# Kernel tuning notes

Hardware: AMD Instinct MI355X
Metric: run time of the kernel (lower is better)

The kernel has to match this reference:

```python
import jax, jax.numpy as jnp
import numpy as np

# Math note: torch does fold(unfold(low_fea,k,pad) * repeat_c(unfold(kernel,1))).
# Because the unfolded low_fea entry at patch (i,j), offset (a,b) is low_fea[c, i-pad+a, j-pad+b],
# fold's overlap-add collapses to: out[n,c,y,x] = low_fea[n,c,y,x] * S[n,y,x], where
#   S[n,y,x] = sum_{a,b in [0,k)} kernel[n, a*k+b, y+pad-a, x+pad-b]  (zero outside bounds).
# We compute S with a zero-padded shifted sum (k*k small static loop) instead of
# materializing the k2*c*h*w unfolded tensor.


def setup_inputs() -> dict:
    key = jax.random.key(0)
    k1, k2 = jax.random.split(key)
    N, K2, C, H, W = 8, 25, 256, 128, 128
    kernel = jax.random.normal(k1, (N, K2, H, W), dtype=jnp.float32)
    low_fea = jax.random.normal(k2, (N, C, H, W), dtype=jnp.float32)
    return {"kernel": kernel, "low_fea": low_fea}


def reference(kernel, low_fea):
    n, c, h, w = low_fea.shape
    k2 = kernel.shape[1]
    k = int(np.sqrt(k2))
    pad = k // 2  # k odd => 2*pad = k-1
    # zero-pad kernel spatially so out-of-bounds taps contribute 0
    Kp = jnp.pad(kernel, ((0, 0), (0, 0), (pad, pad), (pad, pad)))
    # S[n,y,x] = sum_{a,b} kernel[n, a*k+b, y+pad-a, x+pad-b]
    S = jnp.zeros((n, h, w), dtype=low_fea.dtype)
    for a in range(k):
        for b in range(k):
            S = S + Kp[:, a * k + b,
                       2 * pad - a: 2 * pad - a + h,
                       2 * pad - b: 2 * pad - b + w]
    return low_fea * S[:, None, :, :]
```

## Files before the change

### kernel.cpp

```cpp
#include <hip/hip_runtime.h>

#define NN 8
#define CC 256
#define HH 128
#define WW 128
#define KK 5
#define PAD 2

__global__ __launch_bounds__(256) void fused_scale_kernel(
    const float* __restrict__ kern,
    const float* __restrict__ low,
    float* __restrict__ out)
{
    __shared__ __align__(16) float S[WW];

    const int blk = blockIdx.x;
    const int n   = blk >> 7;
    const int y   = blk & (HH - 1);
    const int tid = threadIdx.x;

    if (tid < WW) {
        const int x = tid;
        float s = 0.0f;
        const float* kb = kern + (size_t)n * (KK * KK) * HH * WW;
#pragma unroll
        for (int a = 0; a < KK; ++a) {
            const int yy = y + PAD - a;
            if (yy >= 0 && yy < HH) {
#pragma unroll
                for (int b = 0; b < KK; ++b) {
                    const int xx = x + PAD - b;
                    if (xx >= 0 && xx < WW) {
                        s += kb[((size_t)(a * KK + b) * HH + yy) * WW + xx];
                    }
                }
            }
        }
        S[x] = s;
    }
    __syncthreads();

    const float4* lf4  = (const float4*)low;
    float4*       out4 = (float4*)out;
    const size_t base4 = (((size_t)n * CC * HH + (size_t)y) * WW) >> 2;
    const int    xq    = tid & 31;
    const float4 s4    = *(const float4*)&S[xq * 4];

#pragma unroll 8
    for (int it = 0; it < 32; ++it) {
        const int    c   = it * 8 + (tid >> 5);
        const size_t idx = base4 + (size_t)c * (HH * WW / 4) + (size_t)xq;
        float4 v = lf4[idx];
        float4 r;
        r.x = v.x * s4.x;
        r.y = v.y * s4.y;
        r.z = v.z * s4.z;
        r.w = v.w * s4.w;
        out4[idx] = r;
    }
}

extern "C" void kernel_launch(void* const* d_in, const int* in_sizes, int n_in,
                              void* d_out, int out_size, void* d_ws, size_t ws_size,
                              hipStream_t stream) {
    const float* kern = (const float*)d_in[0];
    const float* low  = (const float*)d_in[1];
    float* out = (float*)d_out;

    dim3 grid(NN * HH);
    dim3 block(256);
    fused_scale_kernel<<<grid, block, 0, stream>>>(kern, low, out);
}
```

Before: 253.9 us.

## Split S computation into separate kernel and parallelize scaling over channel chunks

Computes the per-pixel tap sum S in a dedicated kernel that writes to workspace, then runs a separate scale kernel with eight times more blocks, each handling a 32-channel chunk. This removes the serialized S computation at the head of every streaming block and raises the number of in-flight blocks for the bandwidth-bound multiply. It costs an extra launch and a small round trip of S through global memory, and falls back to the fused kernel when the workspace is too small.

After: 251.2 us. Within noise of the previous version (-1.1%).

```diff
diff --git a/kernel.cpp b/kernel.cpp
--- a/kernel.cpp
+++ b/kernel.cpp
@@ -7,13 +7,72 @@
 #define KK 5
 #define PAD 2
 
+__global__ __launch_bounds__(128) void s_compute_kernel(
+    const float* __restrict__ kern, float* __restrict__ S)
+{
+    const int blk = blockIdx.x;
+    const int n   = blk >> 7;
+    const int y   = blk & (HH - 1);
+    const int x   = threadIdx.x;
+
+    float s = 0.0f;
+    const float* kb = kern + (size_t)n * (KK * KK) * HH * WW;
+#pragma unroll
+    for (int a = 0; a < KK; ++a) {
+        const int yy = y + PAD - a;
+        if (yy >= 0 && yy < HH) {
+#pragma unroll
+            for (int b = 0; b < KK; ++b) {
+                const int xx = x + PAD - b;
+                if (xx >= 0 && xx < WW) {
+                    s += kb[((size_t)(a * KK + b) * HH + yy) * WW + xx];
+                }
+            }
+        }
+    }
+    S[(size_t)blk * WW + x] = s;
+}
+
+__global__ __launch_bounds__(256) void scale_kernel(
+    const float* __restrict__ low,
+    const float* __restrict__ S,
+    float* __restrict__ out)
+{
+    const int blk   = blockIdx.x;
+    const int chunk = blk & 7;
+    const int row   = blk >> 3;
+    const int n     = row >> 7;
+    const int y     = row & (HH - 1);
+    const int tid   = threadIdx.x;
+    const int xq    = tid & 31;
+
+    const float4 s4 = ((const float4*)(S + (size_t)row * WW))[xq];
+
+    const float4* lf4  = (const float4*)low;
+    float4*       out4 = (float4*)out;
+    const size_t base4 = ((size_t)n * CC * HH + (size_t)y) * (WW / 4);
+    const int    c0    = chunk * 32 + (tid >> 5);
+
+#pragma unroll
+    for (int it = 0; it < 4; ++it) {
+        const int    c   = c0 + it * 8;
+        const size_t idx = base4 + (size_t)c * (HH * WW / 4) + (size_t)xq;
+        float4 v = lf4[idx];
+        float4 r;
+        r.x = v.x * s4.x;
+        r.y = v.y * s4.y;
+        r.z = v.z * s4.z;
+        r.w = v.w * s4.w;
+        out4[idx] = r;
+    }
+}
+
 __global__ __launch_bounds__(256) void fused_scale_kernel(
     const float* __restrict__ kern,
     const float* __restrict__ low,
     float* __restrict__ out)
 {
     __shared__ __align__(16) float S[WW];
-
     const int blk = blockIdx.x;
     const int n   = blk >> 7;
     const int y   = blk & (HH - 1);
@@ -67,7 +126,13 @@
     const float* low  = (const float*)d_in[1];
     float* out = (float*)d_out;
 
-    dim3 grid(NN * HH);
-    dim3 block(256);
-    fused_scale_kernel<<<grid, block, 0, stream>>>(kern, low, out);
+    const size_t s_bytes = (size_t)NN * HH * WW * sizeof(float);
+
+    if (ws_size >= s_bytes) {
+        float* S = (float*)d_ws;
+        s_compute_kernel<<<dim3(NN * HH), dim3(128), 0, stream>>>(kern, S);
+        scale_kernel<<<dim3(NN * HH * 8), dim3(256), 0, stream>>>(low, S, out);
+    } else {
+        fused_scale_kernel<<<dim3(NN * HH), dim3(256), 0, stream>>>(kern, low, out);
+    }
 }
```
